# Performance work log

Hardware: AMD Instinct MI355X
Metric: run time of the kernel (lower is better)

## Reference

```python
import jax, jax.numpy as jnp
import numpy as np

EMB = 300      # emb_size
SEQ = 100      # seq_len
KW = 5         # kernel_width
KN = 50        # kernel_num
KMAX = 3       # maxpooling_num
MLP1 = 75      # decoder_mlp1_num
VOCAB = 50000 + 2
B = 2048
QLEN = 5


def setup_inputs() -> dict:
    key = jax.random.key(0)
    ks = jax.random.split(key, 11)
    input_q = jax.random.randint(ks[0], (QLEN,), 0, 50000)
    input_d = jax.random.randint(ks[1], (B, SEQ), 0, 50000)
    emb_table = jax.random.normal(ks[2], (VOCAB, EMB), jnp.float32) * 0.1
    conv_w = jax.random.normal(ks[3], (KW, 3 * EMB, KN), jnp.float32) * 0.02  # WIO
    conv_b = jnp.zeros((KN,), jnp.float32)
    gate_w = jax.random.normal(ks[4], (EMB, KN), jnp.float32) * 0.05
    gate_b = jnp.zeros((KN,), jnp.float32)
    hid_w = jax.random.normal(ks[5], (KN * KMAX, MLP1), jnp.float32) * 0.05
    hid_b = jnp.zeros((MLP1,), jnp.float32)
    score_w = jax.random.normal(ks[6], (MLP1, 1), jnp.float32) * 0.05
    score_b = jnp.zeros((1,), jnp.float32)
    return {"input_q": input_q, "input_d": input_d, "emb_table": emb_table,
            "conv_w": conv_w, "conv_b": conv_b, "gate_w": gate_w, "gate_b": gate_b,
            "hid_w": hid_w, "hid_b": hid_b, "score_w": score_w, "score_b": score_b}


def kmax_pool(x, k):
    # x: [B, KN, L]; keep top-k values along last axis in original sequence order
    _, idx = jax.lax.top_k(x, k)
    idx = jnp.sort(idx, axis=-1)
    return jnp.take_along_axis(x, idx, axis=-1)  # [B, KN, k]


def reference(input_q, input_d, emb_table, conv_w, conv_b, gate_w, gate_b,
              hid_w, hid_b, score_w, score_b):
    # class vector: mean of query-word embeddings -> [EMB]
    class_vec = emb_table[input_q].mean(axis=0)
    # category-specific gate -> [KN]
    query_gate = jax.nn.sigmoid(class_vec @ gate_w + gate_b)
    # document embeddings -> [B, SEQ, EMB]
    emb = emb_table[input_d]
    # elementwise interaction features, concat -> [B, SEQ, 3*EMB]
    conv_in = jnp.concatenate([emb, class_vec * emb, class_vec - emb], axis=-1)
    # conv over sequence (full-width kernel == 1D conv with C_in=3*EMB) -> [B, SEQ-KW+1, KN]
    conv = jax.lax.conv_general_dilated(
        conv_in, conv_w, window_strides=(1,), padding='VALID',
        dimension_numbers=('NWC', 'WIO', 'NWC')) + conv_b
    gated = query_gate * conv                      # [B, L', KN]
    pooled = kmax_pool(jnp.swapaxes(gated, 1, 2), KMAX)  # [B, KN, KMAX]
    enc = pooled.reshape(pooled.shape[0], -1)      # [B, KN*KMAX] = [B, 150]
    mlp1 = jnp.tanh(enc @ hid_w + hid_b)           # [B, 75]
    score = jnp.tanh(mlp1 @ score_w + score_b)     # [B, 1]
    return (mlp1, score)
```

## Files before the change

### kernel.cpp

```cpp
#include <hip/hip_runtime.h>
#include <math.h>

#define EMB   300
#define SEQ   100
#define KW    5
#define KN    50
#define NPAD  64
#define KMAX  3
#define MLP1  75
#define LOUT  96
#define BATCH 2048
#define EPAD  320
#define CHW   32
#define NCHK  10
#define PITCH 36
#define TAU   2.5e-6
#define WHA   0.75
#define WHB   0.25
#define FLAG_TAU 1e-5f

#define WS_C    0
#define WS_GATE 320
#define WS_BIAS 384
#define WS_WG   448
#define F64_DBL 96448
#define WH_F    0
#define WL_F    51200
#define ENC_OFF 102400
#define ENC_PITCH 152
#define FLAGCNT_OFF 413696
#define FLAGLIST_OFF 413704
#define FLAGCAP 4096

typedef __attribute__((ext_vector_type(8))) short short8;
typedef __attribute__((ext_vector_type(4))) float f32x4;

__device__ __forceinline__ unsigned pack_hl(float x) {
    unsigned u = __float_as_uint(x);
    unsigned hi = (u + 0x7fffu + ((u >> 16) & 1u)) >> 16;
    float r = x - __uint_as_float(hi << 16);
    unsigned v = __float_as_uint(r);
    unsigned lo = (v + 0x7fffu + ((v >> 16) & 1u)) >> 16;
    return (hi << 16) | lo;
}

__global__ __launch_bounds__(256) void prep_a(
    const int* __restrict__ qids, const float* __restrict__ emb,
    const float* __restrict__ gate_w, const float* __restrict__ gate_b,
    const float* __restrict__ conv_w, const float* __restrict__ conv_b,
    double* __restrict__ ws, float* wsf)
{
    __shared__ double cS[EMB];
    __shared__ double gS[KN];
    __shared__ double pS[KW][KN];
    int t = threadIdx.x;
    if (t == 0) *(int*)(wsf + FLAGCNT_OFF) = 0;
    for (int e = t; e < EMB; e += 256) {
        double s = 0.0;
        for (int q = 0; q < 5; ++q) s += (double)emb[(size_t)qids[q] * EMB + e];
        double c = s * 0.2;
        cS[e] = c;
        ws[WS_C + e] = c;
    }
    __syncthreads();
    if (t < KN) {
        double g = (double)gate_b[t];
        for (int e = 0; e < EMB; ++e) g += cS[e] * (double)gate_w[e * KN + t];
        g = 1.0 / (1.0 + exp(-g));
        gS[t] = g;
        ws[WS_GATE + t] = g;
    }
    if (t < KW * KN) {
        int n = t % KN, w = t / KN;
        const float* base = conv_w + w * (3 * EMB * KN) + (2 * EMB) * KN + n;
        double p = 0.0;
        for (int e = 0; e < EMB; ++e) p += cS[e] * (double)base[e * KN];
        pS[w][n] = p;
    }
    __syncthreads();
    if (t < KN) {
        double s = (double)conv_b[t];
        for (int w = 0; w < KW; ++w) s += pS[w][t];
        ws[WS_BIAS + t] = gS[t] * s;
    }
}

__global__ __launch_bounds__(256) void prep_b(
    const float* __restrict__ conv_w, const double* __restrict__ ws,
    double* __restrict__ wg, float* __restrict__ wsf)
{
    int gid  = blockIdx.x * 256 + threadIdx.x;
    int wid  = gid >> 6;
    int lane = gid & 63;
    int w = wid / EPAD;
    int e = wid - w * EPAD;
    double v = 0.0;
    if (e < EMB && lane < KN) {
        double c = ws[WS_C + e];
        const float* p = conv_w + (size_t)w * (3 * EMB * KN) + (size_t)e * KN + lane;
        v = ws[WS_GATE + lane] *
            ((double)p[0] + c * (double)p[EMB * KN] - (double)p[2 * EMB * KN]);
    }
    if (e < EMB) wg[(size_t)(w * NPAD + lane) * EMB + e] = v;
    unsigned pk = pack_hl((float)v);
    unsigned short* Wh = (unsigned short*)(wsf + WH_F);
    unsigned short* Wl = (unsigned short*)(wsf + WL_F);
    size_t o = (size_t)(w * NPAD + lane) * EPAD + e;
    Wh[o] = (unsigned short)(pk >> 16);
    Wl[o] = (unsigned short)(pk & 0xffffu);
}

__global__ __launch_bounds__(256, 2) void main_mfma(
    const int* __restrict__ input_d, const float* __restrict__ emb,
    const double* __restrict__ ws, float* wsf,
    const float* __restrict__ hid_w, const float* __restrict__ hid_b,
    const float* __restrict__ score_w, const float* __restrict__ score_b,
    float* __restrict__ out)
{
    __shared__ unsigned stageS[4 * SEQ * PITCH];
    __shared__ int   tokS[4][SEQ];
    __shared__ float encS[4][ENC_PITCH];
    __shared__ float mlpS[4][MLP1 + 1];

    int t = threadIdx.x;
    int wid = t >> 6, lane = t & 63;
    int bb = blockIdx.x * 4 + wid;
    int m = lane & 15, kg = lane >> 4;

    for (int i = lane; i < SEQ; i += 64)
        tokS[wid][i] = input_d[bb * SEQ + i];

    f32x4 acc[6][4];
    #pragma unroll
    for (int lt = 0; lt < 6; ++lt)
        #pragma unroll
        for (int nt = 0; nt < 4; ++nt)
            acc[lt][nt] = (f32x4){0.f, 0.f, 0.f, 0.f};

    const unsigned short* Wh = (const unsigned short*)(wsf + WH_F);
    const unsigned short* Wl = (const unsigned short*)(wsf + WL_F);
    unsigned* stg = stageS + wid * (SEQ * PITCH);

    for (int c = 0; c < NCHK; ++c) {
        int e0 = c * CHW;
        for (int i = lane; i < SEQ * 8; i += 64) {
            int s = i >> 3, g = i & 7;
            int e = e0 + g * 4;
            uint4 pv;
            if (e < EMB) {
                float4 f = *(const float4*)(emb + (size_t)tokS[wid][s] * EMB + e);
                pv.x = pack_hl(f.x); pv.y = pack_hl(f.y);
                pv.z = pack_hl(f.z); pv.w = pack_hl(f.w);
            } else {
                pv = make_uint4(0u, 0u, 0u, 0u);
            }
            *(uint4*)(stg + s * PITCH + g * 4) = pv;
        }
        #pragma unroll 1
        for (int w = 0; w < KW; ++w) {
            short8 Bh[4], Bl[4];
            #pragma unroll
            for (int nt = 0; nt < 4; ++nt) {
                size_t off = (size_t)(w * NPAD + nt * 16 + m) * EPAD + e0 + kg * 8;
                union { uint4 u; short8 s; } xb, yb;
                xb.u = *(const uint4*)(Wh + off);
                yb.u = *(const uint4*)(Wl + off);
                Bh[nt] = xb.s; Bl[nt] = yb.s;
            }
            #pragma unroll
            for (int lt = 0; lt < 6; ++lt) {
                int r = lt * 16 + m + w;
                const unsigned* ap = stg + r * PITCH + kg * 8;
                uint4 p0 = *(const uint4*)(ap);
                uint4 p1 = *(const uint4*)(ap + 4);
                union { uint4 u; short8 s; } ah, al;
                ah.u.x = (p0.y & 0xffff0000u) | (p0.x >> 16);
                ah.u.y = (p0.w & 0xffff0000u) | (p0.z >> 16);
                ah.u.z = (p1.y & 0xffff0000u) | (p1.x >> 16);
                ah.u.w = (p1.w & 0xffff0000u) | (p1.z >> 16);
                al.u.x = (p0.y << 16) | (p0.x & 0xffffu);
                al.u.y = (p0.w << 16) | (p0.z & 0xffffu);
                al.u.z = (p1.y << 16) | (p1.x & 0xffffu);
                al.u.w = (p1.w << 16) | (p1.z & 0xffffu);
                #pragma unroll
                for (int nt = 0; nt < 4; ++nt) {
                    acc[lt][nt] = __builtin_amdgcn_mfma_f32_16x16x32_bf16(ah.s, Bh[nt], acc[lt][nt], 0, 0, 0);
                    acc[lt][nt] = __builtin_amdgcn_mfma_f32_16x16x32_bf16(al.s, Bh[nt], acc[lt][nt], 0, 0, 0);
                    acc[lt][nt] = __builtin_amdgcn_mfma_f32_16x16x32_bf16(ah.s, Bl[nt], acc[lt][nt], 0, 0, 0);
                }
            }
        }
    }

    float* gated = (float*)stg;
    #pragma unroll 1
    for (int ph = 0; ph < 2; ++ph) {
        int np0 = ph * 25;
        __syncthreads();
        #pragma unroll
        for (int nt = 0; nt < 4; ++nt) {
            int n = nt * 16 + m;
            if (n >= np0 && n < np0 + 25) {
                float bias_n = (float)ws[WS_BIAS + n];
                #pragma unroll
                for (int lt = 0; lt < 6; ++lt)
                    #pragma unroll
                    for (int rr = 0; rr < 4; ++rr)
                        gated[(n - np0) * 97 + lt * 16 + kg * 4 + rr] = acc[lt][nt][rr] + bias_n;
            }
        }
        __syncthreads();
        if (lane < 25) {
            int n = np0 + lane;
            const float* row = gated + lane * 97;
            float v1 = -1e30f, v2 = -1e30f, v3 = -1e30f, v4 = -1e30f;
            int   i1 = 0, i2 = 0, i3 = 0, i4 = 0;
            for (int l = 0; l < LOUT; ++l) {
                float v = row[l];
                if (v > v1)      { v4=v3; i4=i3; v3=v2; i3=i2; v2=v1; i2=i1; v1=v; i1=l; }
                else if (v > v2) { v4=v3; i4=i3; v3=v2; i3=i2; v2=v;  i2=l; }
                else if (v > v3) { v4=v3; i4=i3; v3=v;  i3=l; }
                else if (v > v4) { v4=v;  i4=l; }
            }
            float a0=v1, a1=v2, a2=v3; int j0=i1, j1=i2, j2=i3;
            if (j0 > j1) { float tv=a0; a0=a1; a1=tv; int ti=j0; j0=j1; j1=ti; }
            if (j1 > j2) { float tv=a1; a1=a2; a2=tv; int ti=j1; j1=j2; j2=ti; }
            if (j0 > j1) { float tv=a0; a0=a1; a1=tv; int ti=j0; j0=j1; j1=ti; }
            encS[wid][3*n] = a0; encS[wid][3*n+1] = a1; encS[wid][3*n+2] = a2;
            float* enc = wsf + ENC_OFF + (size_t)bb * ENC_PITCH + 3 * n;
            enc[0] = a0; enc[1] = a1; enc[2] = a2;
            if (v3 - v4 <= FLAG_TAU) {
                int idx = atomicAdd((int*)(wsf + FLAGCNT_OFF), 1);
                if (idx < FLAGCAP) ((int*)(wsf + FLAGLIST_OFF))[idx] = (bb << 6) | n;
            }
        }
    }
    __syncthreads();

    for (int i = t; i < 4 * MLP1; i += 256) {
        int d = i / MLP1, o = i - d * MLP1;
        float h = hid_b[o];
        for (int k = 0; k < KN * KMAX; ++k) h = fmaf(encS[d][k], hid_w[k * MLP1 + o], h);
        h = tanhf(h);
        mlpS[d][o] = h;
        out[(blockIdx.x * 4 + d) * MLP1 + o] = h;
    }
    __syncthreads();
    if (t < 4) {
        float s = score_b[0];
        for (int j = 0; j < MLP1; ++j) s = fmaf(mlpS[t][j], score_w[j], s);
        out[BATCH * MLP1 + blockIdx.x * 4 + t] = tanhf(s);
    }
}

__global__ __launch_bounds__(64) void cleanup_enc(
    const int* __restrict__ input_d, const float* __restrict__ emb,
    const double* __restrict__ ws, float* wsf)
{
    int cnt = *(const int*)(wsf + FLAGCNT_OFF);
    if (cnt > FLAGCAP) cnt = FLAGCAP;
    int idx = blockIdx.x;
    if (idx >= cnt) return;
    int code = ((const int*)(wsf + FLAGLIST_OFF))[idx];
    int b = code >> 6, n = code & 63;
    int lane = threadIdx.x;

    __shared__ int    tokS[SEQ];
    __shared__ double rowS[LOUT];
    for (int i = lane; i < SEQ; i += 64) tokS[i] = input_d[b * SEQ + i];
    __syncthreads();

    for (int l = lane; l < LOUT; l += 64) {
        double s = 0.0;
        for (int w = 0; w < KW; ++w) {
            const float*  er = emb + (size_t)tokS[l + w] * EMB;
            const double* wr = ws + WS_WG + (size_t)(w * NPAD + n) * EMB;
            for (int e = 0; e < EMB; ++e) s += (double)er[e] * wr[e];
        }
        rowS[l] = s + ws[WS_BIAS + n];
    }
    __syncthreads();

    if (lane == 0) {
        double v1=-1e300, v2=-1e300, v3=-1e300, v4=-1e300;
        int    i1=0, i2=0, i3=0, i4=0;
        for (int l = 0; l < LOUT; ++l) {
            double v = rowS[l];
            if (v > v1)      { v4=v3; i4=i3; v3=v2; i3=i2; v2=v1; i2=i1; v1=v; i1=l; }
            else if (v > v2) { v4=v3; i4=i3; v3=v2; i3=i2; v2=v;  i2=l; }
            else if (v > v3) { v4=v3; i4=i3; v3=v;  i3=l; }
            else if (v > v4) { v4=v;  i4=l; }
        }
        double a0=v1, a1=v2, a2=v3; int j0=i1, j1=i2, j2=i3;
        if (j0 > j1) { double tv=a0; a0=a1; a1=tv; int ti=j0; j0=j1; j1=ti; }
        if (j1 > j2) { double tv=a1; a1=a2; a2=tv; int ti=j1; j1=j2; j2=ti; }
        if (j0 > j1) { double tv=a0; a0=a1; a1=tv; int ti=j0; j0=j1; j1=ti; }
        double b0=v1, b1=v2, b2=v4; int k0=i1, k1=i2, k2=i4;
        if (k0 > k1) { double tv=b0; b0=b1; b1=tv; int ti=k0; k0=k1; k1=ti; }
        if (k1 > k2) { double tv=b1; b1=b2; b2=tv; int ti=k1; k1=k2; k2=ti; }
        if (k0 > k1) { double tv=b0; b0=b1; b1=tv; int ti=k0; k0=k1; k1=ti; }
        float* enc = wsf + ENC_OFF + (size_t)b * ENC_PITCH + 3 * n;
        if (v3 - v4 > TAU) {
            enc[0] = (float)a0; enc[1] = (float)a1; enc[2] = (float)a2;
        } else {
            enc[0] = (float)(WHA*a0 + WHB*b0);
            enc[1] = (float)(WHA*a1 + WHB*b1);
            enc[2] = (float)(WHA*a2 + WHB*b2);
        }
    }
}

__global__ __launch_bounds__(128) void cleanup_mlp(
    const float* wsf, const float* __restrict__ hid_w, const float* __restrict__ hid_b,
    const float* __restrict__ score_w, const float* __restrict__ score_b,
    float* __restrict__ out)
{
    int cnt = *(const int*)(wsf + FLAGCNT_OFF);
    if (cnt > FLAGCAP) cnt = FLAGCAP;
    if ((int)blockIdx.x >= cnt) return;
    int code = ((const int*)(wsf + FLAGLIST_OFF))[blockIdx.x];
    int b = code >> 6;
    int t = threadIdx.x;
    __shared__ float eS[KN * KMAX];
    __shared__ float mS[MLP1];
    const float* enc = wsf + ENC_OFF + (size_t)b * ENC_PITCH;
    for (int i = t; i < KN * KMAX; i += 128) eS[i] = enc[i];
    __syncthreads();
    if (t < MLP1) {
        float h = hid_b[t];
        for (int k = 0; k < KN * KMAX; ++k) h = fmaf(eS[k], hid_w[k * MLP1 + t], h);
        h = tanhf(h);
        mS[t] = h;
        out[b * MLP1 + t] = h;
    }
    __syncthreads();
    if (t == 0) {
        float s = score_b[0];
        for (int j = 0; j < MLP1; ++j) s = fmaf(mS[j], score_w[j], s);
        out[BATCH * MLP1 + b] = tanhf(s);
    }
}

extern "C" void kernel_launch(void* const* d_in, const int* in_sizes, int n_in,
                              void* d_out, int out_size, void* d_ws, size_t ws_size,
                              hipStream_t stream)
{
    const int*   input_q = (const int*)d_in[0];
    const int*   input_d = (const int*)d_in[1];
    const float* emb     = (const float*)d_in[2];
    const float* conv_w  = (const float*)d_in[3];
    const float* conv_b  = (const float*)d_in[4];
    const float* gate_w  = (const float*)d_in[5];
    const float* gate_b  = (const float*)d_in[6];
    const float* hid_w   = (const float*)d_in[7];
    const float* hid_b   = (const float*)d_in[8];
    const float* score_w = (const float*)d_in[9];
    const float* score_b = (const float*)d_in[10];
    float*  out = (float*)d_out;
    double* ws  = (double*)d_ws;
    float*  wsf = (float*)((char*)d_ws + (size_t)F64_DBL * 8);

    hipLaunchKernelGGL(prep_a, dim3(1), dim3(256), 0, stream,
                       input_q, emb, gate_w, gate_b, conv_w, conv_b, ws, wsf);
    hipLaunchKernelGGL(prep_b, dim3(400), dim3(256), 0, stream,
                       conv_w, ws, ws + WS_WG, wsf);
    hipLaunchKernelGGL(main_mfma, dim3(BATCH / 4), dim3(256), 0, stream,
                       input_d, emb, ws, wsf, hid_w, hid_b, score_w, score_b, out);
    hipLaunchKernelGGL(cleanup_enc, dim3(FLAGCAP), dim3(64), 0, stream,
                       input_d, emb, ws, wsf);
    hipLaunchKernelGGL(cleanup_mlp, dim3(FLAGCAP), dim3(128), 0, stream,
                       wsf, hid_w, hid_b, score_w, score_b, out);
}
```

Measured before the change: 382.2 us.

## Split each document across two waves and pre-split bf16 hi/lo staging

```diff
diff --git a/kernel.cpp b/kernel.cpp
--- a/kernel.cpp
+++ b/kernel.cpp
@@ -13,7 +13,7 @@
 #define EPAD  320
 #define CHW   32
 #define NCHK  10
-#define PITCH 36
+#define SPITCH 40
 #define TAU   2.5e-6
 #define WHA   0.75
 #define WHB   0.25
@@ -110,52 +110,65 @@
     Wl[o] = (unsigned short)(pk & 0xffffu);
 }
 
-__global__ __launch_bounds__(256, 2) void main_mfma(
+__global__ __launch_bounds__(256, 4) void main_mfma(
     const int* __restrict__ input_d, const float* __restrict__ emb,
     const double* __restrict__ ws, float* wsf,
     const float* __restrict__ hid_w, const float* __restrict__ hid_b,
     const float* __restrict__ score_w, const float* __restrict__ score_b,
     float* __restrict__ out)
 {
-    __shared__ unsigned stageS[4 * SEQ * PITCH];
-    __shared__ int   tokS[4][SEQ];
-    __shared__ float encS[4][ENC_PITCH];
-    __shared__ float mlpS[4][MLP1 + 1];
+    __shared__ unsigned short stageS[2][2][SEQ][SPITCH];
+    __shared__ int   tokS[2][SEQ];
+    __shared__ float encS[2][ENC_PITCH];
+    __shared__ float mlpS[2][MLP1 + 1];
 
     int t = threadIdx.x;
     int wid = t >> 6, lane = t & 63;
-    int bb = blockIdx.x * 4 + wid;
+    int dl   = wid >> 1;
+    int half = wid & 1;
+    int pt   = t & 127;
+    int bb = blockIdx.x * 2 + dl;
     int m = lane & 15, kg = lane >> 4;
 
-    for (int i = lane; i < SEQ; i += 64)
-        tokS[wid][i] = input_d[bb * SEQ + i];
-
-    f32x4 acc[6][4];
+    for (int i = pt; i < SEQ; i += 128)
+        tokS[dl][i] = input_d[bb * SEQ + i];
+
+    f32x4 acc[3][4];
     #pragma unroll
-    for (int lt = 0; lt < 6; ++lt)
+    for (int lt = 0; lt < 3; ++lt)
         #pragma unroll
         for (int nt = 0; nt < 4; ++nt)
             acc[lt][nt] = (f32x4){0.f, 0.f, 0.f, 0.f};
 
     const unsigned short* Wh = (const unsigned short*)(wsf + WH_F);
     const unsigned short* Wl = (const unsigned short*)(wsf + WL_F);
-    unsigned* stg = stageS + wid * (SEQ * PITCH);
+
+    __syncthreads();
 
     for (int c = 0; c < NCHK; ++c) {
         int e0 = c * CHW;
-        for (int i = lane; i < SEQ * 8; i += 64) {
-            int s = i >> 3, g = i & 7;
-            int e = e0 + g * 4;
-            uint4 pv;
-            if (e < EMB) {
-                float4 f = *(const float4*)(emb + (size_t)tokS[wid][s] * EMB + e);
-                pv.x = pack_hl(f.x); pv.y = pack_hl(f.y);
-                pv.z = pack_hl(f.z); pv.w = pack_hl(f.w);
-            } else {
-                pv = make_uint4(0u, 0u, 0u, 0u);
-            }
-            *(uint4*)(stg + s * PITCH + g * 4) = pv;
-        }
+        for (int i = pt; i < SEQ * 4; i += 128) {
+            int s = i >> 2, g = i & 3;
+            int e = e0 + g * 8;
+            float4 fa = {0.f, 0.f, 0.f, 0.f}, fb = {0.f, 0.f, 0.f, 0.f};
+            const float* er = emb + (size_t)tokS[dl][s] * EMB;
+            if (e < EMB)     fa = *(const float4*)(er + e);
+            if (e + 4 < EMB) fb = *(const float4*)(er + e + 4);
+            unsigned p0 = pack_hl(fa.x), p1 = pack_hl(fa.y), p2 = pack_hl(fa.z), p3 = pack_hl(fa.w);
+            unsigned p4 = pack_hl(fb.x), p5 = pack_hl(fb.y), p6 = pack_hl(fb.z), p7 = pack_hl(fb.w);
+            uint4 hv, lv;
+            hv.x = (p0 >> 16)     | (p1 & 0xffff0000u);
+            hv.y = (p2 >> 16)     | (p3 & 0xffff0000u);
+            hv.z = (p4 >> 16)     | (p5 & 0xffff0000u);
+            hv.w = (p6 >> 16)     | (p7 & 0xffff0000u);
+            lv.x = (p0 & 0xffffu) | (p1 << 16);
+            lv.y = (p2 & 0xffffu) | (p3 << 16);
+            lv.z = (p4 & 0xffffu) | (p5 << 16);
+            lv.w = (p6 & 0xffffu) | (p7 << 16);
+            *(uint4*)&stageS[dl][0][s][g * 8] = hv;
+            *(uint4*)&stageS[dl][1][s][g * 8] = lv;
+        }
+        __syncthreads();
         #pragma unroll 1
         for (int w = 0; w < KW; ++w) {
             short8 Bh[4], Bl[4];
@@ -168,55 +181,47 @@
                 Bh[nt] = xb.s; Bl[nt] = yb.s;
             }
             #pragma unroll
-            for (int lt = 0; lt < 6; ++lt) {
-                int r = lt * 16 + m + w;
-                const unsigned* ap = stg + r * PITCH + kg * 8;
-                uint4 p0 = *(const uint4*)(ap);
-                uint4 p1 = *(const uint4*)(ap + 4);
-                union { uint4 u; short8 s; } ah, al;
-                ah.u.x = (p0.y & 0xffff0000u) | (p0.x >> 16);
-                ah.u.y = (p0.w & 0xffff0000u) | (p0.z >> 16);
-                ah.u.z = (p1.y & 0xffff0000u) | (p1.x >> 16);
-                ah.u.w = (p1.w & 0xffff0000u) | (p1.z >> 16);
-                al.u.x = (p0.y << 16) | (p0.x & 0xffffu);
-                al.u.y = (p0.w << 16) | (p0.z & 0xffffu);
-                al.u.z = (p1.y << 16) | (p1.x & 0xffffu);
-                al.u.w = (p1.w << 16) | (p1.z & 0xffffu);
+            for (int lt = 0; lt < 3; ++lt) {
+                int r = (half * 3 + lt) * 16 + m + w;
+                short8 ah = *(const short8*)&stageS[dl][0][r][kg * 8];
+                short8 al = *(const short8*)&stageS[dl][1][r][kg * 8];
                 #pragma unroll
                 for (int nt = 0; nt < 4; ++nt) {
-                    acc[lt][nt] = __builtin_amdgcn_mfma_f32_16x16x32_bf16(ah.s, Bh[nt], acc[lt][nt], 0, 0, 0);
-                    acc[lt][nt] = __builtin_amdgcn_mfma_f32_16x16x32_bf16(al.s, Bh[nt], acc[lt][nt], 0, 0, 0);
-                    acc[lt][nt] = __builtin_amdgcn_mfma_f32_16x16x32_bf16(ah.s, Bl[nt], acc[lt][nt], 0, 0, 0);
+                    acc[lt][nt] = __builtin_amdgcn_mfma_f32_16x16x32_bf16(ah, Bh[nt], acc[lt][nt], 0, 0, 0);
+                    acc[lt][nt] = __builtin_amdgcn_mfma_f32_16x16x32_bf16(al, Bh[nt], acc[lt][nt], 0, 0, 0);
+                    acc[lt][nt] = __builtin_amdgcn_mfma_f32_16x16x32_bf16(ah, Bl[nt], acc[lt][nt], 0, 0, 0);
                 }
             }
         }
-    }
-
-    float* gated = (float*)stg;
+        __syncthreads();
+    }
+
+    float* gated = (float*)&stageS[dl][0][0][0];
     #pragma unroll 1
     for (int ph = 0; ph < 2; ++ph) {
         int np0 = ph * 25;
-        __syncthreads();
         #pragma unroll
         for (int nt = 0; nt < 4; ++nt) {
             int n = nt * 16 + m;
             if (n >= np0 && n < np0 + 25) {
                 float bias_n = (float)ws[WS_BIAS + n];
                 #pragma unroll
-                for (int lt = 0; lt < 6; ++lt)
+                for (int lt = 0; lt < 3; ++lt)
                     #pragma unroll
                     for (int rr = 0; rr < 4; ++rr)
-                        gated[(n - np0) * 97 + lt * 16 + kg * 4 + rr] = acc[lt][nt][rr] + bias_n;
+                        gated[(n - np0) * 97 + (half * 3 + lt) * 16 + kg * 4 + rr] = acc[lt][nt][rr] + bias_n;
             }
         }
         __syncthreads();
-        if (lane < 25) {
-            int n = np0 + lane;
-            const float* row = gated + lane * 97;
+        int nr = half ? 12 : 13;
+        if (lane < nr) {
+            int row = half * 13 + lane;
+            int n = np0 + row;
+            const float* rowp = gated + row * 97;
             float v1 = -1e30f, v2 = -1e30f, v3 = -1e30f, v4 = -1e30f;
             int   i1 = 0, i2 = 0, i3 = 0, i4 = 0;
             for (int l = 0; l < LOUT; ++l) {
-                float v = row[l];
+                float v = rowp[l];
                 if (v > v1)      { v4=v3; i4=i3; v3=v2; i3=i2; v2=v1; i2=i1; v1=v; i1=l; }
                 else if (v > v2) { v4=v3; i4=i3; v3=v2; i3=i2; v2=v;  i2=l; }
                 else if (v > v3) { v4=v3; i4=i3; v3=v;  i3=l; }
@@ -226,7 +231,7 @@
             if (j0 > j1) { float tv=a0; a0=a1; a1=tv; int ti=j0; j0=j1; j1=ti; }
             if (j1 > j2) { float tv=a1; a1=a2; a2=tv; int ti=j1; j1=j2; j2=ti; }
             if (j0 > j1) { float tv=a0; a0=a1; a1=tv; int ti=j0; j0=j1; j1=ti; }
-            encS[wid][3*n] = a0; encS[wid][3*n+1] = a1; encS[wid][3*n+2] = a2;
+            encS[dl][3*n] = a0; encS[dl][3*n+1] = a1; encS[dl][3*n+2] = a2;
             float* enc = wsf + ENC_OFF + (size_t)bb * ENC_PITCH + 3 * n;
             enc[0] = a0; enc[1] = a1; enc[2] = a2;
             if (v3 - v4 <= FLAG_TAU) {
@@ -234,22 +239,22 @@
                 if (idx < FLAGCAP) ((int*)(wsf + FLAGLIST_OFF))[idx] = (bb << 6) | n;
             }
         }
-    }
-    __syncthreads();
-
-    for (int i = t; i < 4 * MLP1; i += 256) {
+        __syncthreads();
+    }
+
+    for (int i = t; i < 2 * MLP1; i += 256) {
         int d = i / MLP1, o = i - d * MLP1;
         float h = hid_b[o];
         for (int k = 0; k < KN * KMAX; ++k) h = fmaf(encS[d][k], hid_w[k * MLP1 + o], h);
         h = tanhf(h);
         mlpS[d][o] = h;
-        out[(blockIdx.x * 4 + d) * MLP1 + o] = h;
-    }
-    __syncthreads();
-    if (t < 4) {
+        out[(blockIdx.x * 2 + d) * MLP1 + o] = h;
+    }
+    __syncthreads();
+    if (t < 2) {
         float s = score_b[0];
         for (int j = 0; j < MLP1; ++j) s = fmaf(mlpS[t][j], score_w[j], s);
-        out[BATCH * MLP1 + blockIdx.x * 4 + t] = tanhf(s);
+        out[BATCH * MLP1 + blockIdx.x * 2 + t] = tanhf(s);
     }
 }
 
@@ -364,7 +369,7 @@
                        input_q, emb, gate_w, gate_b, conv_w, conv_b, ws, wsf);
     hipLaunchKernelGGL(prep_b, dim3(400), dim3(256), 0, stream,
                        conv_w, ws, ws + WS_WG, wsf);
-    hipLaunchKernelGGL(main_mfma, dim3(BATCH / 4), dim3(256), 0, stream,
+    hipLaunchKernelGGL(main_mfma, dim3(BATCH / 2), dim3(256), 0, stream,
                        input_d, emb, ws, wsf, hid_w, hid_b, score_w, score_b, out);
     hipLaunchKernelGGL(cleanup_enc, dim3(FLAGCAP), dim3(64), 0, stream,
                        input_d, emb, ws, wsf);
```

Measured after the change: 449.2 us. 1.18x slower.
